# Optimization experiments

Measured on AMD Instinct MI355X. Metric: run time of the kernel, lower is better.

## Reference

```python
import jax, jax.numpy as jnp
import numpy as np

B = 65536
IN = 256
H = 256
COMB = IN + H


def setup_inputs() -> dict:
    key = jax.random.key(0)
    ks = jax.random.split(key, 11)
    s_in = 1.0 / np.sqrt(COMB)
    inp = {
        "x_t": jax.random.normal(ks[0], (B, IN), dtype=jnp.float32),
        "h_prev": jax.random.normal(ks[1], (B, H), dtype=jnp.float32),
        "c_prev": jax.random.normal(ks[2], (B, H), dtype=jnp.float32),
        # nn.Linear weights: [out, in] layout, uniform(-1/sqrt(in), 1/sqrt(in))
        "W_f": jax.random.uniform(ks[3], (H, COMB), jnp.float32, -s_in, s_in),
        "b_f": jax.random.uniform(ks[4], (H,), jnp.float32, -s_in, s_in),
        "W_i": jax.random.uniform(ks[5], (H, COMB), jnp.float32, -s_in, s_in),
        "b_i": jax.random.uniform(ks[6], (H,), jnp.float32, -s_in, s_in),
        "W_o": jax.random.uniform(ks[7], (H, COMB), jnp.float32, -s_in, s_in),
        "b_o": jax.random.uniform(ks[8], (H,), jnp.float32, -s_in, s_in),
        "W_g": jax.random.uniform(ks[9], (H, COMB), jnp.float32, -s_in, s_in),
        "b_g": jax.random.uniform(ks[10], (H,), jnp.float32, -s_in, s_in),
    }
    return inp


def reference(x_t, h_prev, c_prev, W_f, b_f, W_i, b_i, W_o, b_o, W_g, b_g):
    combined = jnp.concatenate([x_t, h_prev], axis=-1)  # [B, COMB]
    # Stack the four gate weights into one GEMM: [B, COMB] @ [COMB, 4H]
    W = jnp.concatenate([W_f, W_i, W_o, W_g], axis=0)   # [4H, COMB]
    b = jnp.concatenate([b_f, b_i, b_o, b_g], axis=0)   # [4H]
    gates = combined @ W.T + b                           # [B, 4H]
    f_lin, i_lin, o_lin, g_lin = jnp.split(gates, 4, axis=-1)
    f_t = jax.nn.sigmoid(f_lin)
    i_t = jax.nn.sigmoid(i_lin)
    o_t = jax.nn.sigmoid(o_lin)
    g_t = jnp.tanh(g_lin)
    c_t = f_t * c_prev + i_t * g_t
    h_t = o_t * jnp.tanh(c_t)
    return (h_t, c_t, f_t, i_t, o_t, g_t)
```

## Files before the change

kernel.cpp:

```cpp
#include <hip/hip_runtime.h>
#include <cstdint>
#include <cstddef>

#define B_SZ 65536

typedef __attribute__((ext_vector_type(8))) short bf16x8;
typedef __attribute__((ext_vector_type(8))) unsigned short u16x8;
typedef __attribute__((ext_vector_type(4))) float f32x4;

__device__ __forceinline__ unsigned short f2bf(float f) {
  union { float f; uint32_t u; } v; v.f = f;
  uint32_t u = v.u;
  uint32_t r = (u + 0x7FFFu + ((u >> 16) & 1u)) >> 16;
  return (unsigned short)r;
}

__global__ __launch_bounds__(256) void pack_w_kernel(const float* __restrict__ Wf,
                                                     const float* __restrict__ Wi,
                                                     const float* __restrict__ Wo,
                                                     const float* __restrict__ Wg,
                                                     unsigned short* __restrict__ out) {
  int i = blockIdx.x * 256 + threadIdx.x;
  int rho = i >> 6, c = i & 63;
  int bn = rho >> 8;
  int r = rho & 255;
  int wc = r >> 6, gate = (r >> 4) & 3, hh = r & 15;
  int srow = (bn << 6) + (wc << 4) + hh;
  const float* W = (gate == 0) ? Wf : (gate == 1) ? Wi : (gate == 2) ? Wo : Wg;
  const float* src = W + (size_t)srow * 512 + ((size_t)c << 3);
  float4 v0 = ((const float4*)src)[0];
  float4 v1 = ((const float4*)src)[1];
  u16x8 o;
  o[0] = f2bf(v0.x); o[1] = f2bf(v0.y); o[2] = f2bf(v0.z); o[3] = f2bf(v0.w);
  o[4] = f2bf(v1.x); o[5] = f2bf(v1.y); o[6] = f2bf(v1.z); o[7] = f2bf(v1.w);
  *((u16x8*)(out + ((size_t)i << 3))) = o;
}

__device__ __forceinline__ float sigmoid_f(float x) {
  return __builtin_amdgcn_rcpf(1.f + __expf(-x));
}
__device__ __forceinline__ float tanh_f(float x) {
  return 1.f - 2.f * __builtin_amdgcn_rcpf(__expf(2.f * x) + 1.f);
}

__global__ __launch_bounds__(512, 2) void lstm_fused_kernel(
    const float* __restrict__ X, const float* __restrict__ Hp,
    const unsigned short* __restrict__ Wb, const float* __restrict__ c_prev,
    const float* __restrict__ bf_, const float* __restrict__ bi_,
    const float* __restrict__ bo_, const float* __restrict__ bg_,
    float* __restrict__ out) {
  __shared__ __align__(16) unsigned short As[2][128 * 64];
  __shared__ __align__(16) unsigned short Bs[2][256 * 64];

  const int L = blockIdx.x;
  const int xcd = L & 7, slot = L >> 3;
  const int mt = (xcd << 6) + (slot >> 2);
  const int bn = slot & 3;
  const int m0 = mt << 7;

  const int t = threadIdx.x;
  const int lane = t & 63, w = t >> 6;
  const int r15 = lane & 15, quad = lane >> 4;
  const int mbase = (w >> 2) << 6;
  const int nbase = (w & 3) << 6;

  const int h = (bn << 6) + ((w & 3) << 4) + r15;
  const float Bf = bf_[h], Bi = bi_[h], Bo = bo_[h], Bg = bg_[h];

  const int la0 = t, la1 = t + 512;
  const int ar0 = la0 >> 3, ar1 = la1 >> 3;
  const int ac0 = (la0 & 7) ^ (ar0 & 7), ac1 = (la1 & 7) ^ (ar1 & 7);

  f32x4 zero = {0.f, 0.f, 0.f, 0.f};
  f32x4 acc[4][4];
#pragma unroll
  for (int a = 0; a < 4; ++a)
#pragma unroll
    for (int b = 0; b < 4; ++b) acc[a][b] = zero;

  float4 av[4];

  auto load_A = [&](int kt) {
    const float* src = (kt < 4) ? X : Hp;
    const int kcol = (kt & 3) << 6;
    const float* p0 = src + (size_t)(m0 + ar0) * 256 + kcol + (ac0 << 3);
    const float* p1 = src + (size_t)(m0 + ar1) * 256 + kcol + (ac1 << 3);
    av[0] = ((const float4*)p0)[0];
    av[1] = ((const float4*)p0)[1];
    av[2] = ((const float4*)p1)[0];
    av[3] = ((const float4*)p1)[1];
  };

  auto write_A = [&](int buf) {
    u16x8 o0, o1;
    o0[0] = f2bf(av[0].x); o0[1] = f2bf(av[0].y); o0[2] = f2bf(av[0].z); o0[3] = f2bf(av[0].w);
    o0[4] = f2bf(av[1].x); o0[5] = f2bf(av[1].y); o0[6] = f2bf(av[1].z); o0[7] = f2bf(av[1].w);
    o1[0] = f2bf(av[2].x); o1[1] = f2bf(av[2].y); o1[2] = f2bf(av[2].z); o1[3] = f2bf(av[2].w);
    o1[4] = f2bf(av[3].x); o1[5] = f2bf(av[3].y); o1[6] = f2bf(av[3].z); o1[7] = f2bf(av[3].w);
    *((u16x8*)&As[buf][la0 << 3]) = o0;
    *((u16x8*)&As[buf][la1 << 3]) = o1;
  };

  auto stage_B = [&](int buf, int kt) {
    const int k0 = kt << 6;
#pragma unroll
    for (int jj = 0; jj < 4; ++jj) {
      int l = (jj << 9) + t;
      int row = l >> 3, st = l & 7;
      int c = st ^ (row & 7);
      const unsigned short* gb =
          Wb + (size_t)((bn << 8) + row) * 512 + k0 + (c << 3);
      __builtin_amdgcn_global_load_lds(
          (const __attribute__((address_space(1))) void*)gb,
          (__attribute__((address_space(3))) void*)(&Bs[buf][l << 3]), 16, 0, 0);
    }
  };

  auto compute = [&](int buf) {
#pragma unroll
    for (int ks = 0; ks < 2; ++ks) {
      bf16x8 af[4], bfr[4];
      const int ch = (ks << 2) + quad;
#pragma unroll
      for (int mi = 0; mi < 4; ++mi) {
        int row = mbase + (mi << 4) + r15;
        af[mi] = *((const bf16x8*)&As[buf][(row << 6) + ((ch ^ (row & 7)) << 3)]);
      }
#pragma unroll
      for (int gi = 0; gi < 4; ++gi) {
        int row = nbase + (gi << 4) + r15;
        bfr[gi] = *((const bf16x8*)&Bs[buf][(row << 6) + ((ch ^ (row & 7)) << 3)]);
      }
#pragma unroll
      for (int mi = 0; mi < 4; ++mi)
#pragma unroll
        for (int gi = 0; gi < 4; ++gi)
          acc[mi][gi] = __builtin_amdgcn_mfma_f32_16x16x32_bf16(
              af[mi], bfr[gi], acc[mi][gi], 0, 0, 0);
    }
  };

  load_A(0);
  stage_B(0, 0);
  write_A(0);
  __syncthreads();

#pragma unroll
  for (int kt = 0; kt < 8; ++kt) {
    const int cur = kt & 1, nxt = cur ^ 1;
    if (kt < 7) {
      load_A(kt + 1);
      stage_B(nxt, kt + 1);
    }
    compute(cur);
    if (kt < 7) write_A(nxt);
    __syncthreads();
  }

  const size_t S = (size_t)B_SZ * 256;
#pragma unroll
  for (int mi = 0; mi < 4; ++mi) {
    const int mr0 = m0 + mbase + (mi << 4) + (quad << 2);
#pragma unroll
    for (int r = 0; r < 4; ++r) {
      const int m = mr0 + r;
      float F = acc[mi][0][r] + Bf;
      float I = acc[mi][1][r] + Bi;
      float O = acc[mi][2][r] + Bo;
      float G = acc[mi][3][r] + Bg;
      float f = sigmoid_f(F);
      float ii = sigmoid_f(I);
      float o = sigmoid_f(O);
      float g = tanh_f(G);
      size_t base = (size_t)m * 256 + h;
      float cp = c_prev[base];
      float ct = f * cp + ii * g;
      float ht = o * tanh_f(ct);
      out[base] = ht;
      out[S + base] = ct;
      out[2 * S + base] = f;
      out[3 * S + base] = ii;
      out[4 * S + base] = o;
      out[5 * S + base] = g;
    }
  }
}

extern "C" void kernel_launch(void* const* d_in, const int* in_sizes, int n_in,
                              void* d_out, int out_size, void* d_ws, size_t ws_size,
                              hipStream_t stream) {
  const float* x   = (const float*)d_in[0];
  const float* hp  = (const float*)d_in[1];
  const float* cp  = (const float*)d_in[2];
  const float* Wf  = (const float*)d_in[3];
  const float* bf_ = (const float*)d_in[4];
  const float* Wi  = (const float*)d_in[5];
  const float* bi_ = (const float*)d_in[6];
  const float* Wo  = (const float*)d_in[7];
  const float* bo_ = (const float*)d_in[8];
  const float* Wg  = (const float*)d_in[9];
  const float* bg_ = (const float*)d_in[10];
  float* out = (float*)d_out;

  unsigned short* Wb = (unsigned short*)d_ws;

  pack_w_kernel<<<dim3(256), dim3(256), 0, stream>>>(Wf, Wi, Wo, Wg, Wb);
  lstm_fused_kernel<<<dim3(2048), dim3(512), 0, stream>>>(x, hp, Wb, cp, bf_, bi_,
                                                          bo_, bg_, out);
}
```

Measured before the change: 640.2 us.

## Halve K-tile to 32 to cut LDS and raise occupancy to four blocks

Shrinks the K-step of the double-buffered pipeline from 64 to 32. This halves the shared-memory footprint from 96KB to 48KB per block, so the launch bound can request 4 blocks per CU instead of 2. The LDS swizzle is rewritten for 4-chunk rows, and the main loop now runs 16 iterations instead of 8. This trades twice as many barriers and loads per block, plus tighter register limits (possible spills with 64 accumulator floats), for more latency hiding from the extra resident waves.

```diff
diff --git a/kernel.cpp b/kernel.cpp
--- a/kernel.cpp
+++ b/kernel.cpp
@@ -43,14 +43,14 @@
   return 1.f - 2.f * __builtin_amdgcn_rcpf(__expf(2.f * x) + 1.f);
 }
 
-__global__ __launch_bounds__(512, 2) void lstm_fused_kernel(
+__global__ __launch_bounds__(512, 4) void lstm_fused_kernel(
     const float* __restrict__ X, const float* __restrict__ Hp,
     const unsigned short* __restrict__ Wb, const float* __restrict__ c_prev,
     const float* __restrict__ bf_, const float* __restrict__ bi_,
     const float* __restrict__ bo_, const float* __restrict__ bg_,
     float* __restrict__ out) {
-  __shared__ __align__(16) unsigned short As[2][128 * 64];
-  __shared__ __align__(16) unsigned short Bs[2][256 * 64];
+  __shared__ __align__(16) unsigned short As[2][128 * 32];
+  __shared__ __align__(16) unsigned short Bs[2][256 * 32];
 
   const int L = blockIdx.x;
   const int xcd = L & 7, slot = L >> 3;
@@ -67,9 +67,8 @@
   const int h = (bn << 6) + ((w & 3) << 4) + r15;
   const float Bf = bf_[h], Bi = bi_[h], Bo = bo_[h], Bg = bg_[h];
 
-  const int la0 = t, la1 = t + 512;
-  const int ar0 = la0 >> 3, ar1 = la1 >> 3;
-  const int ac0 = (la0 & 7) ^ (ar0 & 7), ac1 = (la1 & 7) ^ (ar1 & 7);
+  const int ar = t >> 2, as_ = t & 3;
+  const int ac = as_ ^ ((ar >> 1) & 3);
 
   f32x4 zero = {0.f, 0.f, 0.f, 0.f};
   f32x4 acc[4][4];
@@ -78,36 +77,30 @@
 #pragma unroll
     for (int b = 0; b < 4; ++b) acc[a][b] = zero;
 
-  float4 av[4];
+  float4 av0, av1;
 
   auto load_A = [&](int kt) {
-    const float* src = (kt < 4) ? X : Hp;
-    const int kcol = (kt & 3) << 6;
-    const float* p0 = src + (size_t)(m0 + ar0) * 256 + kcol + (ac0 << 3);
-    const float* p1 = src + (size_t)(m0 + ar1) * 256 + kcol + (ac1 << 3);
-    av[0] = ((const float4*)p0)[0];
-    av[1] = ((const float4*)p0)[1];
-    av[2] = ((const float4*)p1)[0];
-    av[3] = ((const float4*)p1)[1];
+    const float* src = (kt < 8) ? X : Hp;
+    const int kcol = (kt & 7) << 5;
+    const float* p = src + (size_t)(m0 + ar) * 256 + kcol + (ac << 3);
+    av0 = ((const float4*)p)[0];
+    av1 = ((const float4*)p)[1];
   };
 
   auto write_A = [&](int buf) {
-    u16x8 o0, o1;
-    o0[0] = f2bf(av[0].x); o0[1] = f2bf(av[0].y); o0[2] = f2bf(av[0].z); o0[3] = f2bf(av[0].w);
-    o0[4] = f2bf(av[1].x); o0[5] = f2bf(av[1].y); o0[6] = f2bf(av[1].z); o0[7] = f2bf(av[1].w);
-    o1[0] = f2bf(av[2].x); o1[1] = f2bf(av[2].y); o1[2] = f2bf(av[2].z); o1[3] = f2bf(av[2].w);
-    o1[4] = f2bf(av[3].x); o1[5] = f2bf(av[3].y); o1[6] = f2bf(av[3].z); o1[7] = f2bf(av[3].w);
-    *((u16x8*)&As[buf][la0 << 3]) = o0;
-    *((u16x8*)&As[buf][la1 << 3]) = o1;
+    u16x8 o;
+    o[0] = f2bf(av0.x); o[1] = f2bf(av0.y); o[2] = f2bf(av0.z); o[3] = f2bf(av0.w);
+    o[4] = f2bf(av1.x); o[5] = f2bf(av1.y); o[6] = f2bf(av1.z); o[7] = f2bf(av1.w);
+    *((u16x8*)&As[buf][t << 3]) = o;
   };
 
   auto stage_B = [&](int buf, int kt) {
-    const int k0 = kt << 6;
-#pragma unroll
-    for (int jj = 0; jj < 4; ++jj) {
+    const int k0 = kt << 5;
+#pragma unroll
+    for (int jj = 0; jj < 2; ++jj) {
       int l = (jj << 9) + t;
-      int row = l >> 3, st = l & 7;
-      int c = st ^ (row & 7);
+      int row = l >> 2, st = l & 3;
+      int c = st ^ ((row >> 1) & 3);
       const unsigned short* gb =
           Wb + (size_t)((bn << 8) + row) * 512 + k0 + (c << 3);
       __builtin_amdgcn_global_load_lds(
@@ -117,27 +110,25 @@
   };
 
   auto compute = [&](int buf) {
-#pragma unroll
-    for (int ks = 0; ks < 2; ++ks) {
-      bf16x8 af[4], bfr[4];
-      const int ch = (ks << 2) + quad;
-#pragma unroll
-      for (int mi = 0; mi < 4; ++mi) {
-        int row = mbase + (mi << 4) + r15;
-        af[mi] = *((const bf16x8*)&As[buf][(row << 6) + ((ch ^ (row & 7)) << 3)]);
-      }
-#pragma unroll
-      for (int gi = 0; gi < 4; ++gi) {
-        int row = nbase + (gi << 4) + r15;
-        bfr[gi] = *((const bf16x8*)&Bs[buf][(row << 6) + ((ch ^ (row & 7)) << 3)]);
-      }
-#pragma unroll
-      for (int mi = 0; mi < 4; ++mi)
-#pragma unroll
-        for (int gi = 0; gi < 4; ++gi)
-          acc[mi][gi] = __builtin_amdgcn_mfma_f32_16x16x32_bf16(
-              af[mi], bfr[gi], acc[mi][gi], 0, 0, 0);
-    }
+    bf16x8 af[4], bfr[4];
+#pragma unroll
+    for (int mi = 0; mi < 4; ++mi) {
+      int row = mbase + (mi << 4) + r15;
+      int sl = quad ^ ((row >> 1) & 3);
+      af[mi] = *((const bf16x8*)&As[buf][(row << 5) + (sl << 3)]);
+    }
+#pragma unroll
+    for (int gi = 0; gi < 4; ++gi) {
+      int row = nbase + (gi << 4) + r15;
+      int sl = quad ^ ((row >> 1) & 3);
+      bfr[gi] = *((const bf16x8*)&Bs[buf][(row << 5) + (sl << 3)]);
+    }
+#pragma unroll
+    for (int mi = 0; mi < 4; ++mi)
+#pragma unroll
+      for (int gi = 0; gi < 4; ++gi)
+        acc[mi][gi] = __builtin_amdgcn_mfma_f32_16x16x32_bf16(
+            af[mi], bfr[gi], acc[mi][gi], 0, 0, 0);
   };
 
   load_A(0);
@@ -146,14 +137,14 @@
   __syncthreads();
 
 #pragma unroll
-  for (int kt = 0; kt < 8; ++kt) {
+  for (int kt = 0; kt < 16; ++kt) {
     const int cur = kt & 1, nxt = cur ^ 1;
-    if (kt < 7) {
+    if (kt < 15) {
       load_A(kt + 1);
       stage_B(nxt, kt + 1);
     }
     compute(cur);
-    if (kt < 7) write_A(nxt);
+    if (kt < 15) write_A(nxt);
     __syncthreads();
   }
 
```

Result: slower. 710.3 us (+10.9%).
